# Kernel tuning notes

Measured on AMD Instinct MI355X. Metric: run time of the kernel, lower is better.

## Reference

```python
import jax, jax.numpy as jnp
import numpy as np

B, T, C = 4, 2048, 1024
H, E = 4096, 8


def setup_inputs() -> dict:
    key = jax.random.key(0)
    ks = jax.random.split(key, 6)
    scale = 0.02
    x = jax.random.normal(ks[0], (B, T, C), dtype=jnp.float32)
    w_router = jax.random.normal(ks[1], (C, E), dtype=jnp.float32) * scale
    b_router = jnp.zeros((E,), dtype=jnp.float32)
    w1 = jax.random.normal(ks[2], (E, C, H), dtype=jnp.float32) * scale
    b1 = jnp.zeros((E, H), dtype=jnp.float32)
    w2 = jax.random.normal(ks[3], (E, H, C), dtype=jnp.float32) * scale
    b2 = jnp.zeros((E, C), dtype=jnp.float32)
    return {"x": x, "w_router": w_router, "b_router": b_router,
            "w1": w1, "b1": b1, "w2": w2, "b2": b2}


def reference(x, w_router, b_router, w1, b1, w2, b2):
    # Router: logits -> softmax -> top-1 expert index per token
    logits = jnp.einsum('btc,ce->bte', x, w_router) + b_router  # [B,T,E]
    probs = jax.nn.softmax(logits, axis=-1)
    top1 = jnp.argmax(probs, axis=-1)  # [B,T] int

    # Per-expert dense MLP, combined via top-1 mask (masked scatter in torch).
    out = jnp.zeros_like(x)
    for e in range(E):
        h = jax.nn.gelu(jnp.einsum('btc,ch->bth', x, w1[e]) + b1[e],
                        approximate=False)           # [B,T,H]
        y = jnp.einsum('bth,hc->btc', h, w2[e]) + b2[e]  # [B,T,C]
        out = out + jnp.where((top1 == e)[..., None], y, 0.0)
    return out
```

## Files before the change

### kernel.cpp

```cpp
#include <hip/hip_runtime.h>
#include <cstdint>
#include <cstddef>

#define NTOK 8192
#define C_ 1024
#define H_ 4096
#define E_ 8
#define YMAX2 72

typedef __attribute__((ext_vector_type(8))) short short8;
typedef __attribute__((ext_vector_type(4))) float f32x4;
typedef __attribute__((ext_vector_type(4))) unsigned int u32x4;

__device__ __forceinline__ uint16_t f2b(float f) {
    uint32_t x;
    __builtin_memcpy(&x, &f, 4);
    x = (x + 0x7fffu + ((x >> 16) & 1u)) >> 16;
    return (uint16_t)x;
}

__device__ __forceinline__ float gelu_f(float v) {
    float u = v * (0.7978845608028654f + 0.03567740814183f * v * v);
    float t = __expf(2.f * u);
    float th = 1.f - 2.f / (t + 1.f);
    return 0.5f * v * (1.f + th);
}

__global__ __launch_bounds__(256) void router_kernel(
    const float* __restrict__ x, const float* __restrict__ wr,
    const float* __restrict__ br, int* __restrict__ top1)
{
    int wid = threadIdx.x >> 6, lane = threadIdx.x & 63;
    int tok = blockIdx.x * 4 + wid;
    const float* xrow = x + (size_t)tok * C_;
    float acc[E_];
#pragma unroll
    for (int e = 0; e < E_; e++) acc[e] = 0.f;
#pragma unroll 4
    for (int i = 0; i < C_ / 64; i++) {
        int c = i * 64 + lane;
        float xv = xrow[c];
        const f32x4 w0 = *(const f32x4*)(wr + (size_t)c * E_);
        const f32x4 w1v = *(const f32x4*)(wr + (size_t)c * E_ + 4);
#pragma unroll
        for (int e = 0; e < 4; e++) acc[e] += xv * w0[e];
#pragma unroll
        for (int e = 0; e < 4; e++) acc[4 + e] += xv * w1v[e];
    }
#pragma unroll
    for (int off = 32; off > 0; off >>= 1) {
#pragma unroll
        for (int e = 0; e < E_; e++) acc[e] += __shfl_xor(acc[e], off, 64);
    }
    if (lane == 0) {
        float best = acc[0] + br[0];
        int bi = 0;
#pragma unroll
        for (int e = 1; e < E_; e++) {
            float v = acc[e] + br[e];
            if (v > best) { best = v; bi = e; }
        }
        top1[tok] = bi;
    }
}

__global__ void zero_counts(int* counts) {
    if (threadIdx.x < E_) counts[threadIdx.x] = 0;
}

__global__ __launch_bounds__(1024) void scatter_kernel(
    const int* __restrict__ top1, int* counts, int* __restrict__ idx)
{
    __shared__ int lc[E_], base[E_];
    int tid = threadIdx.x;
    if (tid < E_) lc[tid] = 0;
    __syncthreads();
    int t = blockIdx.x * 1024 + tid;
    int e = top1[t];
    int my = atomicAdd(&lc[e], 1);
    __syncthreads();
    if (tid < E_) base[tid] = atomicAdd(&counts[tid], lc[tid]);
    __syncthreads();
    idx[e * NTOK + base[e] + my] = t;
}

__global__ void plan_kernel(const int* __restrict__ counts,
                            int* __restrict__ tab2, int* __restrict__ ranges2)
{
    if (threadIdx.x == 0) {
        int n = 0, n0 = 0;
        for (int e = 0; e < E_; e++) {
            int nt = (counts[e] + 127) >> 7;
            for (int mb = 0; mb < nt; mb++) tab2[n++] = (e << 16) | mb;
            if (e == 3) n0 = n;
        }
        ranges2[0] = 0;  ranges2[1] = n;
        ranges2[2] = 0;  ranges2[3] = n0;
        ranges2[4] = n0; ranges2[5] = n;
    }
}

__global__ __launch_bounds__(256) void convert_x_kernel(
    const float* __restrict__ x, uint16_t* __restrict__ xb)
{
    size_t i = ((size_t)blockIdx.x * 256 + threadIdx.x) * 8;
    f32x4 a = *(const f32x4*)(x + i);
    f32x4 b = *(const f32x4*)(x + i + 4);
    u32x4 o;
    o.x = (uint32_t)f2b(a.x) | ((uint32_t)f2b(a.y) << 16);
    o.y = (uint32_t)f2b(a.z) | ((uint32_t)f2b(a.w) << 16);
    o.z = (uint32_t)f2b(b.x) | ((uint32_t)f2b(b.y) << 16);
    o.w = (uint32_t)f2b(b.z) | ((uint32_t)f2b(b.w) << 16);
    *(u32x4*)(xb + i) = o;
}

__global__ __launch_bounds__(256) void transpose_cvt_kernel(
    const float* __restrict__ w, uint16_t* __restrict__ wt,
    int K, int N, int ebase)
{
    __shared__ uint16_t tile[64][66];
    int ez = blockIdx.z, e = ebase + ez;
    int n0 = blockIdx.x * 64, k0 = blockIdx.y * 64;
    int t = threadIdx.x;
#pragma unroll
    for (int i = 0; i < 4; i++) {
        int chunk = i * 256 + t;
        int r = chunk >> 4, c4 = chunk & 15;
        f32x4 v = *(const f32x4*)(w + (size_t)(e * K + k0 + r) * N + n0 + c4 * 4);
        uint32_t u0 = (uint32_t)f2b(v.x) | ((uint32_t)f2b(v.y) << 16);
        uint32_t u1 = (uint32_t)f2b(v.z) | ((uint32_t)f2b(v.w) << 16);
        *(uint32_t*)&tile[r][c4 * 4 + 0] = u0;
        *(uint32_t*)&tile[r][c4 * 4 + 2] = u1;
    }
    __syncthreads();
#pragma unroll
    for (int i = 0; i < 2; i++) {
        int chunk = i * 256 + t;
        int rn = chunk >> 3, ck = chunk & 7;
        uint32_t p[4];
#pragma unroll
        for (int j = 0; j < 4; j++) {
            uint32_t lo = tile[ck * 8 + 2 * j][rn];
            uint32_t hi = tile[ck * 8 + 2 * j + 1][rn];
            p[j] = lo | (hi << 16);
        }
        u32x4 v; v.x = p[0]; v.y = p[1]; v.z = p[2]; v.w = p[3];
        *(u32x4*)(wt + ((size_t)ez * N + n0 + rn) * K + k0 + ck * 8) = v;
    }
}

template <int YB, int K, int N, typename OutT, bool GELU>
__global__ __launch_bounds__(256, 3) void gemm_kernel(
    const uint16_t* __restrict__ A, const uint16_t* __restrict__ Bt,
    const float* __restrict__ bias, OutT* __restrict__ Out,
    const int* __restrict__ counts, const int* __restrict__ idx,
    const int* __restrict__ tab, const int* __restrict__ range, int ebase)
{
    constexpr int BM = 128, BN = 128, NW = 256;
    constexpr int MR = 4;
    constexpr int NITER = K / 32;
    constexpr int GX = N / BN;
    constexpr int NWG = GX * YB;
    static_assert(NWG % 8 == 0, "grid must be divisible by 8 XCDs");

    int o = blockIdx.y * GX + blockIdx.x;
    int lid = (o & 7) * (NWG / 8) + (o >> 3);
    int nb = lid % GX;
    int tile = range[0] + lid / GX;
    if (tile >= range[1]) return;
    int ent = tab[tile];
    int e = ent >> 16, mb = ent & 0xffff;
    int ez = e - ebase;
    int cnt = counts[e];

    __shared__ __align__(16) uint16_t As[BM][32];
    __shared__ __align__(16) uint16_t Bs[BN][32];

    int t = threadIdx.x;
    int lane = t & 63, w = t >> 6;
    int wm = w >> 1, wn = w & 1;

    const int* idxe = idx + e * NTOK;

    f32x4 acc[MR][4];
#pragma unroll
    for (int mt = 0; mt < MR; mt++)
#pragma unroll
        for (int nt = 0; nt < 4; nt++) acc[mt][nt] = (f32x4)(0.f);

    const uint16_t* Bte = Bt + ((size_t)ez * N + (size_t)nb * BN) * K;
    uint16_t* As0 = &As[0][0];
    uint16_t* Bs0 = &Bs[0][0];

    const uint16_t* aptr[2];
    const uint16_t* bptr[2];
    uint16_t* adst[2];
    uint16_t* bdst[2];
#pragma unroll
    for (int i = 0; i < 2; i++) {
        int cid = i * NW + t;
        int r = cid >> 2, j = cid & 3;
        int s = mb * BM + r;
        int tk = idxe[(s < cnt) ? s : 0];
        aptr[i] = A + (size_t)tk * K + (j ^ ((r >> 1) & 3)) * 8;
        adst[i] = As0 + (size_t)cid * 8;
    }
#pragma unroll
    for (int i = 0; i < 2; i++) {
        int cid = i * NW + t;
        int r = cid >> 2, j = cid & 3;
        bptr[i] = Bte + (size_t)r * K + (j ^ ((r >> 1) & 3)) * 8;
        bdst[i] = Bs0 + (size_t)cid * 8;
    }

    u32x4 ra[2], rb[2];
    auto loadreg = [&](int kt) {
        int k0 = kt * 32;
#pragma unroll
        for (int i = 0; i < 2; i++) ra[i] = *(const u32x4*)(aptr[i] + k0);
#pragma unroll
        for (int i = 0; i < 2; i++) rb[i] = *(const u32x4*)(bptr[i] + k0);
    };
    auto ldswrite = [&]() {
#pragma unroll
        for (int i = 0; i < 2; i++) *(u32x4*)adst[i] = ra[i];
#pragma unroll
        for (int i = 0; i < 2; i++) *(u32x4*)bdst[i] = rb[i];
    };

    int cs = (((lane >> 4) ^ ((lane & 15) >> 1)) & 3) * 8;

    auto compute = [&]() {
        short8 af[MR], bf[4];
#pragma unroll
        for (int mt = 0; mt < MR; mt++)
            af[mt] = *(const short8*)
                (As0 + (wm * 64 + mt * 16 + (lane & 15)) * 32 + cs);
#pragma unroll
        for (int nt = 0; nt < 4; nt++)
            bf[nt] = *(const short8*)
                (Bs0 + (wn * 64 + nt * 16 + (lane & 15)) * 32 + cs);
#pragma unroll
        for (int mt = 0; mt < MR; mt++)
#pragma unroll
            for (int nt = 0; nt < 4; nt++)
                acc[mt][nt] = __builtin_amdgcn_mfma_f32_16x16x32_bf16(
                    af[mt], bf[nt], acc[mt][nt], 0, 0, 0);
    };

    loadreg(0);
    ldswrite();
    __syncthreads();

    for (int kt = 0; kt < NITER - 1; ++kt) {
        loadreg(kt + 1);
        __builtin_amdgcn_sched_barrier(0);
        compute();
        __syncthreads();
        ldswrite();
        __syncthreads();
    }
    compute();

    const float* be = bias + (size_t)e * N;
#pragma unroll
    for (int mt = 0; mt < MR; mt++) {
        int rbase = wm * 64 + mt * 16 + (lane >> 4) * 4;
#pragma unroll
        for (int r = 0; r < 4; r++) {
            int row = rbase + r;
            int s = mb * BM + row;
            if (s < cnt) {
                int tk = idxe[s];
#pragma unroll
                for (int nt = 0; nt < 4; nt++) {
                    int gcol = nb * BN + wn * 64 + nt * 16 + (lane & 15);
                    float v = acc[mt][nt][r] + be[gcol];
                    if (GELU) v = gelu_f(v);
                    if constexpr (sizeof(OutT) == 2)
                        Out[(size_t)tk * N + gcol] = (OutT)f2b(v);
                    else
                        Out[(size_t)tk * N + gcol] = v;
                }
            }
        }
    }
}

extern "C" void kernel_launch(void* const* d_in, const int* in_sizes, int n_in,
                              void* d_out, int out_size, void* d_ws, size_t ws_size,
                              hipStream_t stream)
{
    const float* x  = (const float*)d_in[0];
    const float* wr = (const float*)d_in[1];
    const float* br = (const float*)d_in[2];
    const float* b1 = (const float*)d_in[4];
    const float* w1 = (const float*)d_in[3];
    const float* w2 = (const float*)d_in[5];
    const float* b2 = (const float*)d_in[6];
    float* out = (float*)d_out;

    char* ws = (char*)d_ws;
    int* counts    = (int*)ws;
    int* top1      = (int*)(ws + 1024);
    int* idx       = (int*)(ws + 64 * 1024);
    int* tab2      = (int*)(ws + 392 * 1024);
    int* ranges2   = (int*)(ws + 396 * 1024);
    uint16_t* xb   = (uint16_t*)(ws + ((size_t)1 << 20));
    uint16_t* hbuf = (uint16_t*)(ws + ((size_t)17 << 20));
    uint16_t* wT   = (uint16_t*)(ws + ((size_t)81 << 20));

    bool big = ws_size >= ((size_t)145 << 20);

    hipLaunchKernelGGL(zero_counts, dim3(1), dim3(64), 0, stream, counts);
    hipLaunchKernelGGL(router_kernel, dim3(NTOK / 4), dim3(256), 0, stream,
                       x, wr, br, top1);
    hipLaunchKernelGGL(scatter_kernel, dim3(NTOK / 1024), dim3(1024), 0, stream,
                       top1, counts, idx);
    hipLaunchKernelGGL(plan_kernel, dim3(1), dim3(64), 0, stream,
                       counts, tab2, ranges2);
    hipLaunchKernelGGL(convert_x_kernel, dim3(NTOK * C_ / (256 * 8)), dim3(256), 0,
                       stream, x, xb);

    if (big) {
        hipLaunchKernelGGL(transpose_cvt_kernel, dim3(H_ / 64, C_ / 64, E_),
                           dim3(256), 0, stream, w1, wT, C_, H_, 0);
        hipLaunchKernelGGL((gemm_kernel<YMAX2, C_, H_, uint16_t, true>),
                           dim3(H_ / 128, YMAX2, 1), dim3(256), 0, stream,
                           xb, wT, b1, hbuf, counts, idx, tab2, ranges2, 0);
        hipLaunchKernelGGL(transpose_cvt_kernel, dim3(C_ / 64, H_ / 64, E_),
                           dim3(256), 0, stream, w2, wT, H_, C_, 0);
        hipLaunchKernelGGL((gemm_kernel<YMAX2, H_, C_, float, false>),
                           dim3(C_ / 128, YMAX2, 1), dim3(256), 0, stream,
                           hbuf, wT, b2, out, counts, idx, tab2, ranges2, 0);
    } else {
        for (int c = 0; c < 2; c++) {
            hipLaunchKernelGGL(transpose_cvt_kernel, dim3(H_ / 64, C_ / 64, 4),
                               dim3(256), 0, stream, w1, wT, C_, H_, c * 4);
            hipLaunchKernelGGL((gemm_kernel<YMAX2, C_, H_, uint16_t, true>),
                               dim3(H_ / 128, YMAX2, 1), dim3(256), 0, stream,
                               xb, wT, b1, hbuf, counts, idx, tab2, ranges2 + 2 + 2 * c, c * 4);
        }
        for (int c = 0; c < 2; c++) {
            hipLaunchKernelGGL(transpose_cvt_kernel, dim3(C_ / 64, H_ / 64, 4),
                               dim3(256), 0, stream, w2, wT, H_, C_, c * 4);
            hipLaunchKernelGGL((gemm_kernel<YMAX2, H_, C_, float, false>),
                               dim3(C_ / 128, YMAX2, 1), dim3(256), 0, stream,
                               hbuf, wT, b2, out, counts, idx, tab2, ranges2 + 2 + 2 * c, c * 4);
        }
    }
}
```

Measured before the change: 570.2 us.

## Template GEMM tile shape and use 256x256x64 tiles for first expert GEMM

```diff
diff --git a/kernel.cpp b/kernel.cpp
--- a/kernel.cpp
+++ b/kernel.cpp
@@ -6,6 +6,7 @@
 #define C_ 1024
 #define H_ 4096
 #define E_ 8
+#define YMAX1 40
 #define YMAX2 72
 
 typedef __attribute__((ext_vector_type(8))) short short8;
@@ -85,10 +86,21 @@
 }
 
 __global__ void plan_kernel(const int* __restrict__ counts,
+                            int* __restrict__ tab1, int* __restrict__ ranges1,
                             int* __restrict__ tab2, int* __restrict__ ranges2)
 {
     if (threadIdx.x == 0) {
         int n = 0, n0 = 0;
+        for (int e = 0; e < E_; e++) {
+            int nt = (counts[e] + 255) >> 8;
+            for (int mb = 0; mb < nt; mb++) tab1[n++] = (e << 16) | mb;
+            if (e == 3) n0 = n;
+        }
+        ranges1[0] = 0;  ranges1[1] = n;
+        ranges1[2] = 0;  ranges1[3] = n0;
+        ranges1[4] = n0; ranges1[5] = n;
+
+        n = 0; n0 = 0;
         for (int e = 0; e < E_; e++) {
             int nt = (counts[e] + 127) >> 7;
             for (int mb = 0; mb < nt; mb++) tab2[n++] = (e << 16) | mb;
@@ -149,19 +161,25 @@
     }
 }
 
-template <int YB, int K, int N, typename OutT, bool GELU>
-__global__ __launch_bounds__(256, 3) void gemm_kernel(
+template <int BM, int BN, int BK, int NW, int WM, int WN, int MINW,
+          int YB, int K, int N, typename OutT, bool GELU>
+__global__ __launch_bounds__(NW, MINW) void gemm_kernel(
     const uint16_t* __restrict__ A, const uint16_t* __restrict__ Bt,
     const float* __restrict__ bias, OutT* __restrict__ Out,
     const int* __restrict__ counts, const int* __restrict__ idx,
     const int* __restrict__ tab, const int* __restrict__ range, int ebase)
 {
-    constexpr int BM = 128, BN = 128, NW = 256;
-    constexpr int MR = 4;
-    constexpr int NITER = K / 32;
+    constexpr int MR = BM / (WM * 16);
+    constexpr int NT = BN / (WN * 16);
+    constexpr int CPR = BK / 8;
+    constexpr int AI = BM * BK / (8 * NW);
+    constexpr int BI = BN * BK / (8 * NW);
+    constexpr int KS = BK / 32;
+    constexpr int NITER = K / BK;
     constexpr int GX = N / BN;
     constexpr int NWG = GX * YB;
     static_assert(NWG % 8 == 0, "grid must be divisible by 8 XCDs");
+    static_assert(CPR == 4 || CPR == 8, "BK must be 32 or 64");
 
     int o = blockIdx.y * GX + blockIdx.x;
     int lid = (o & 7) * (NWG / 8) + (o >> 3);
@@ -173,79 +191,83 @@
     int ez = e - ebase;
     int cnt = counts[e];
 
-    __shared__ __align__(16) uint16_t As[BM][32];
-    __shared__ __align__(16) uint16_t Bs[BN][32];
+    __shared__ __align__(16) uint16_t As[BM][BK];
+    __shared__ __align__(16) uint16_t Bs[BN][BK];
 
     int t = threadIdx.x;
     int lane = t & 63, w = t >> 6;
-    int wm = w >> 1, wn = w & 1;
+    int wm = w / WN, wn = w % WN;
 
     const int* idxe = idx + e * NTOK;
 
-    f32x4 acc[MR][4];
+    f32x4 acc[MR][NT];
 #pragma unroll
     for (int mt = 0; mt < MR; mt++)
 #pragma unroll
-        for (int nt = 0; nt < 4; nt++) acc[mt][nt] = (f32x4)(0.f);
+        for (int nt = 0; nt < NT; nt++) acc[mt][nt] = (f32x4)(0.f);
 
     const uint16_t* Bte = Bt + ((size_t)ez * N + (size_t)nb * BN) * K;
     uint16_t* As0 = &As[0][0];
     uint16_t* Bs0 = &Bs[0][0];
 
-    const uint16_t* aptr[2];
-    const uint16_t* bptr[2];
-    uint16_t* adst[2];
-    uint16_t* bdst[2];
-#pragma unroll
-    for (int i = 0; i < 2; i++) {
+    const uint16_t* aptr[AI];
+    const uint16_t* bptr[BI];
+#pragma unroll
+    for (int i = 0; i < AI; i++) {
         int cid = i * NW + t;
-        int r = cid >> 2, j = cid & 3;
+        int r = cid / CPR, j = cid % CPR;
+        int sw = (CPR == 8) ? (r & 7) : ((r >> 1) & 3);
         int s = mb * BM + r;
         int tk = idxe[(s < cnt) ? s : 0];
-        aptr[i] = A + (size_t)tk * K + (j ^ ((r >> 1) & 3)) * 8;
-        adst[i] = As0 + (size_t)cid * 8;
-    }
-#pragma unroll
-    for (int i = 0; i < 2; i++) {
+        aptr[i] = A + (size_t)tk * K + (j ^ sw) * 8;
+    }
+#pragma unroll
+    for (int i = 0; i < BI; i++) {
         int cid = i * NW + t;
-        int r = cid >> 2, j = cid & 3;
-        bptr[i] = Bte + (size_t)r * K + (j ^ ((r >> 1) & 3)) * 8;
-        bdst[i] = Bs0 + (size_t)cid * 8;
-    }
-
-    u32x4 ra[2], rb[2];
+        int r = cid / CPR, j = cid % CPR;
+        int sw = (CPR == 8) ? (r & 7) : ((r >> 1) & 3);
+        bptr[i] = Bte + (size_t)r * K + (j ^ sw) * 8;
+    }
+
+    u32x4 ra[AI], rb[BI];
     auto loadreg = [&](int kt) {
-        int k0 = kt * 32;
-#pragma unroll
-        for (int i = 0; i < 2; i++) ra[i] = *(const u32x4*)(aptr[i] + k0);
-#pragma unroll
-        for (int i = 0; i < 2; i++) rb[i] = *(const u32x4*)(bptr[i] + k0);
+        int k0 = kt * BK;
+#pragma unroll
+        for (int i = 0; i < AI; i++) ra[i] = *(const u32x4*)(aptr[i] + k0);
+#pragma unroll
+        for (int i = 0; i < BI; i++) rb[i] = *(const u32x4*)(bptr[i] + k0);
     };
     auto ldswrite = [&]() {
 #pragma unroll
-        for (int i = 0; i < 2; i++) *(u32x4*)adst[i] = ra[i];
-#pragma unroll
-        for (int i = 0; i < 2; i++) *(u32x4*)bdst[i] = rb[i];
+        for (int i = 0; i < AI; i++) *(u32x4*)(As0 + (size_t)(i * NW + t) * 8) = ra[i];
+#pragma unroll
+        for (int i = 0; i < BI; i++) *(u32x4*)(Bs0 + (size_t)(i * NW + t) * 8) = rb[i];
     };
 
-    int cs = (((lane >> 4) ^ ((lane & 15) >> 1)) & 3) * 8;
-
     auto compute = [&]() {
-        short8 af[MR], bf[4];
-#pragma unroll
-        for (int mt = 0; mt < MR; mt++)
-            af[mt] = *(const short8*)
-                (As0 + (wm * 64 + mt * 16 + (lane & 15)) * 32 + cs);
-#pragma unroll
-        for (int nt = 0; nt < 4; nt++)
-            bf[nt] = *(const short8*)
-                (Bs0 + (wn * 64 + nt * 16 + (lane & 15)) * 32 + cs);
-#pragma unroll
-        for (int mt = 0; mt < MR; mt++)
-#pragma unroll
-            for (int nt = 0; nt < 4; nt++)
-                acc[mt][nt] = __builtin_amdgcn_mfma_f32_16x16x32_bf16(
-                    af[mt], bf[nt], acc[mt][nt], 0, 0, 0);
+#pragma unroll
+        for (int ks = 0; ks < KS; ks++) {
+            int cs;
+            if constexpr (CPR == 8)
+                cs = (((ks * 4 + (lane >> 4)) ^ (lane & 7)) & 7) * 8;
+            else
+                cs = (((lane >> 4) ^ ((lane & 15) >> 1)) & 3) * 8;
+            short8 af[MR], bf[NT];
+#pragma unroll
+            for (int mt = 0; mt < MR; mt++)
+                af[mt] = *(const short8*)
+                    (As0 + (wm * (BM / WM) + mt * 16 + (lane & 15)) * BK + cs);
+#pragma unroll
+            for (int nt = 0; nt < NT; nt++)
+                bf[nt] = *(const short8*)
+                    (Bs0 + (wn * (BN / WN) + nt * 16 + (lane & 15)) * BK + cs);
+#pragma unroll
+            for (int mt = 0; mt < MR; mt++)
+#pragma unroll
+                for (int nt = 0; nt < NT; nt++)
+                    acc[mt][nt] = __builtin_amdgcn_mfma_f32_16x16x32_bf16(
+                        af[mt], bf[nt], acc[mt][nt], 0, 0, 0);
+        }
     };
 
     loadreg(0);
@@ -265,7 +287,7 @@
     const float* be = bias + (size_t)e * N;
 #pragma unroll
     for (int mt = 0; mt < MR; mt++) {
-        int rbase = wm * 64 + mt * 16 + (lane >> 4) * 4;
+        int rbase = wm * (BM / WM) + mt * 16 + (lane >> 4) * 4;
 #pragma unroll
         for (int r = 0; r < 4; r++) {
             int row = rbase + r;
@@ -273,8 +295,8 @@
             if (s < cnt) {
                 int tk = idxe[s];
 #pragma unroll
-                for (int nt = 0; nt < 4; nt++) {
-                    int gcol = nb * BN + wn * 64 + nt * 16 + (lane & 15);
+                for (int nt = 0; nt < NT; nt++) {
+                    int gcol = nb * BN + wn * (BN / WN) + nt * 16 + (lane & 15);
                     float v = acc[mt][nt][r] + be[gcol];
                     if (GELU) v = gelu_f(v);
                     if constexpr (sizeof(OutT) == 2)
@@ -304,6 +326,8 @@
     int* counts    = (int*)ws;
     int* top1      = (int*)(ws + 1024);
     int* idx       = (int*)(ws + 64 * 1024);
+    int* tab1      = (int*)(ws + 384 * 1024);
+    int* ranges1   = (int*)(ws + 388 * 1024);
     int* tab2      = (int*)(ws + 392 * 1024);
     int* ranges2   = (int*)(ws + 396 * 1024);
     uint16_t* xb   = (uint16_t*)(ws + ((size_t)1 << 20));
@@ -318,33 +342,37 @@
     hipLaunchKernelGGL(scatter_kernel, dim3(NTOK / 1024), dim3(1024), 0, stream,
                        top1, counts, idx);
     hipLaunchKernelGGL(plan_kernel, dim3(1), dim3(64), 0, stream,
-                       counts, tab2, ranges2);
+                       counts, tab1, ranges1, tab2, ranges2);
     hipLaunchKernelGGL(convert_x_kernel, dim3(NTOK * C_ / (256 * 8)), dim3(256), 0,
                        stream, x, xb);
 
     if (big) {
         hipLaunchKernelGGL(transpose_cvt_kernel, dim3(H_ / 64, C_ / 64, E_),
                            dim3(256), 0, stream, w1, wT, C_, H_, 0);
-        hipLaunchKernelGGL((gemm_kernel<YMAX2, C_, H_, uint16_t, true>),
-                           dim3(H_ / 128, YMAX2, 1), dim3(256), 0, stream,
-                           xb, wT, b1, hbuf, counts, idx, tab2, ranges2, 0);
+        hipLaunchKernelGGL((gemm_kernel<256, 256, 64, 512, 2, 4, 2,
+                                        YMAX1, C_, H_, uint16_t, true>),
+                           dim3(H_ / 256, YMAX1, 1), dim3(512), 0, stream,
+                           xb, wT, b1, hbuf, counts, idx, tab1, ranges1, 0);
         hipLaunchKernelGGL(transpose_cvt_kernel, dim3(C_ / 64, H_ / 64, E_),
                            dim3(256), 0, stream, w2, wT, H_, C_, 0);
-        hipLaunchKernelGGL((gemm_kernel<YMAX2, H_, C_, float, false>),
+        hipLaunchKernelGGL((gemm_kernel<128, 128, 32, 256, 2, 2, 6,
+                                        YMAX2, H_, C_, float, false>),
                            dim3(C_ / 128, YMAX2, 1), dim3(256), 0, stream,
                            hbuf, wT, b2, out, counts, idx, tab2, ranges2, 0);
     } else {
         for (int c = 0; c < 2; c++) {
             hipLaunchKernelGGL(transpose_cvt_kernel, dim3(H_ / 64, C_ / 64, 4),
                                dim3(256), 0, stream, w1, wT, C_, H_, c * 4);
-            hipLaunchKernelGGL((gemm_kernel<YMAX2, C_, H_, uint16_t, true>),
-                               dim3(H_ / 128, YMAX2, 1), dim3(256), 0, stream,
-                               xb, wT, b1, hbuf, counts, idx, tab2, ranges2 + 2 + 2 * c, c * 4);
+            hipLaunchKernelGGL((gemm_kernel<256, 256, 64, 512, 2, 4, 2,
+                                            YMAX1, C_, H_, uint16_t, true>),
+                               dim3(H_ / 256, YMAX1, 1), dim3(512), 0, stream,
+                               xb, wT, b1, hbuf, counts, idx, tab1, ranges1 + 2 + 2 * c, c * 4);
         }
         for (int c = 0; c < 2; c++) {
             hipLaunchKernelGGL(transpose_cvt_kernel, dim3(C_ / 64, H_ / 64, 4),
                                dim3(256), 0, stream, w2, wT, H_, C_, c * 4);
-            hipLaunchKernelGGL((gemm_kernel<YMAX2, H_, C_, float, false>),
+            hipLaunchKernelGGL((gemm_kernel<128, 128, 32, 256, 2, 2, 6,
+                                            YMAX2, H_, C_, float, false>),
                                dim3(C_ / 128, YMAX2, 1), dim3(256), 0, stream,
                                hbuf, wT, b2, out, counts, idx, tab2, ranges2 + 2 + 2 * c, c * 4);
         }
```

After: 1.291 ms. 2.26x slower.

## Double-buffer GEMM LDS tiles, fuse x bf16 conversion into router, reorder tile mapping

Applied to the files above, without the earlier changes.

```diff
diff --git a/kernel.cpp b/kernel.cpp
--- a/kernel.cpp
+++ b/kernel.cpp
@@ -6,7 +6,7 @@
 #define C_ 1024
 #define H_ 4096
 #define E_ 8
-#define YMAX2 72
+#define YMAX 72
 
 typedef __attribute__((ext_vector_type(8))) short short8;
 typedef __attribute__((ext_vector_type(4))) float f32x4;
@@ -28,11 +28,13 @@
 
 __global__ __launch_bounds__(256) void router_kernel(
     const float* __restrict__ x, const float* __restrict__ wr,
-    const float* __restrict__ br, int* __restrict__ top1)
+    const float* __restrict__ br, int* __restrict__ top1,
+    uint16_t* __restrict__ xb)
 {
     int wid = threadIdx.x >> 6, lane = threadIdx.x & 63;
     int tok = blockIdx.x * 4 + wid;
     const float* xrow = x + (size_t)tok * C_;
+    uint16_t* xbrow = xb + (size_t)tok * C_;
     float acc[E_];
 #pragma unroll
     for (int e = 0; e < E_; e++) acc[e] = 0.f;
@@ -40,6 +42,7 @@
     for (int i = 0; i < C_ / 64; i++) {
         int c = i * 64 + lane;
         float xv = xrow[c];
+        xbrow[c] = f2b(xv);
         const f32x4 w0 = *(const f32x4*)(wr + (size_t)c * E_);
         const f32x4 w1v = *(const f32x4*)(wr + (size_t)c * E_ + 4);
 #pragma unroll
@@ -85,33 +88,19 @@
 }
 
 __global__ void plan_kernel(const int* __restrict__ counts,
-                            int* __restrict__ tab2, int* __restrict__ ranges2)
+                            int* __restrict__ tab, int* __restrict__ ranges)
 {
     if (threadIdx.x == 0) {
         int n = 0, n0 = 0;
         for (int e = 0; e < E_; e++) {
             int nt = (counts[e] + 127) >> 7;
-            for (int mb = 0; mb < nt; mb++) tab2[n++] = (e << 16) | mb;
+            for (int mb = 0; mb < nt; mb++) tab[n++] = (e << 16) | mb;
             if (e == 3) n0 = n;
         }
-        ranges2[0] = 0;  ranges2[1] = n;
-        ranges2[2] = 0;  ranges2[3] = n0;
-        ranges2[4] = n0; ranges2[5] = n;
-    }
-}
-
-__global__ __launch_bounds__(256) void convert_x_kernel(
-    const float* __restrict__ x, uint16_t* __restrict__ xb)
-{
-    size_t i = ((size_t)blockIdx.x * 256 + threadIdx.x) * 8;
-    f32x4 a = *(const f32x4*)(x + i);
-    f32x4 b = *(const f32x4*)(x + i + 4);
-    u32x4 o;
-    o.x = (uint32_t)f2b(a.x) | ((uint32_t)f2b(a.y) << 16);
-    o.y = (uint32_t)f2b(a.z) | ((uint32_t)f2b(a.w) << 16);
-    o.z = (uint32_t)f2b(b.x) | ((uint32_t)f2b(b.y) << 16);
-    o.w = (uint32_t)f2b(b.z) | ((uint32_t)f2b(b.w) << 16);
-    *(u32x4*)(xb + i) = o;
+        ranges[0] = 0;  ranges[1] = n;
+        ranges[2] = 0;  ranges[3] = n0;
+        ranges[4] = n0; ranges[5] = n;
+    }
 }
 
 __global__ __launch_bounds__(256) void transpose_cvt_kernel(
@@ -162,19 +151,20 @@
     constexpr int GX = N / BN;
     constexpr int NWG = GX * YB;
     static_assert(NWG % 8 == 0, "grid must be divisible by 8 XCDs");
-
-    int o = blockIdx.y * GX + blockIdx.x;
+    static_assert((NITER & 1) == 0, "NITER must be even");
+
+    int o = blockIdx.x * YB + blockIdx.y;
     int lid = (o & 7) * (NWG / 8) + (o >> 3);
-    int nb = lid % GX;
-    int tile = range[0] + lid / GX;
+    int nb = lid / YB;
+    int tile = range[0] + lid % YB;
     if (tile >= range[1]) return;
     int ent = tab[tile];
     int e = ent >> 16, mb = ent & 0xffff;
     int ez = e - ebase;
     int cnt = counts[e];
 
-    __shared__ __align__(16) uint16_t As[BM][32];
-    __shared__ __align__(16) uint16_t Bs[BN][32];
+    __shared__ __align__(16) uint16_t As[2][BM][32];
+    __shared__ __align__(16) uint16_t Bs[2][BN][32];
 
     int t = threadIdx.x;
     int lane = t & 63, w = t >> 6;
@@ -189,13 +179,9 @@
         for (int nt = 0; nt < 4; nt++) acc[mt][nt] = (f32x4)(0.f);
 
     const uint16_t* Bte = Bt + ((size_t)ez * N + (size_t)nb * BN) * K;
-    uint16_t* As0 = &As[0][0];
-    uint16_t* Bs0 = &Bs[0][0];
 
     const uint16_t* aptr[2];
     const uint16_t* bptr[2];
-    uint16_t* adst[2];
-    uint16_t* bdst[2];
 #pragma unroll
     for (int i = 0; i < 2; i++) {
         int cid = i * NW + t;
@@ -203,14 +189,12 @@
         int s = mb * BM + r;
         int tk = idxe[(s < cnt) ? s : 0];
         aptr[i] = A + (size_t)tk * K + (j ^ ((r >> 1) & 3)) * 8;
-        adst[i] = As0 + (size_t)cid * 8;
     }
 #pragma unroll
     for (int i = 0; i < 2; i++) {
         int cid = i * NW + t;
         int r = cid >> 2, j = cid & 3;
         bptr[i] = Bte + (size_t)r * K + (j ^ ((r >> 1) & 3)) * 8;
-        bdst[i] = Bs0 + (size_t)cid * 8;
     }
 
     u32x4 ra[2], rb[2];
@@ -221,25 +205,27 @@
 #pragma unroll
         for (int i = 0; i < 2; i++) rb[i] = *(const u32x4*)(bptr[i] + k0);
     };
-    auto ldswrite = [&]() {
-#pragma unroll
-        for (int i = 0; i < 2; i++) *(u32x4*)adst[i] = ra[i];
-#pragma unroll
-        for (int i = 0; i < 2; i++) *(u32x4*)bdst[i] = rb[i];
+    auto ldswrite = [&](int sel) {
+#pragma unroll
+        for (int i = 0; i < 2; i++)
+            *(u32x4*)(&As[sel][0][0] + (size_t)(i * NW + t) * 8) = ra[i];
+#pragma unroll
+        for (int i = 0; i < 2; i++)
+            *(u32x4*)(&Bs[sel][0][0] + (size_t)(i * NW + t) * 8) = rb[i];
     };
 
     int cs = (((lane >> 4) ^ ((lane & 15) >> 1)) & 3) * 8;
 
-    auto compute = [&]() {
+    auto compute = [&](int sel) {
         short8 af[MR], bf[4];
 #pragma unroll
         for (int mt = 0; mt < MR; mt++)
             af[mt] = *(const short8*)
-                (As0 + (wm * 64 + mt * 16 + (lane & 15)) * 32 + cs);
+                (&As[sel][0][0] + (wm * 64 + mt * 16 + (lane & 15)) * 32 + cs);
 #pragma unroll
         for (int nt = 0; nt < 4; nt++)
             bf[nt] = *(const short8*)
-                (Bs0 + (wn * 64 + nt * 16 + (lane & 15)) * 32 + cs);
+                (&Bs[sel][0][0] + (wn * 64 + nt * 16 + (lane & 15)) * 32 + cs);
 #pragma unroll
         for (int mt = 0; mt < MR; mt++)
 #pragma unroll
@@ -249,18 +235,27 @@
     };
 
     loadreg(0);
-    ldswrite();
-    __syncthreads();
-
-    for (int kt = 0; kt < NITER - 1; ++kt) {
+    ldswrite(0);
+    __syncthreads();
+
+    for (int kt = 0; kt + 2 < NITER; kt += 2) {
         loadreg(kt + 1);
         __builtin_amdgcn_sched_barrier(0);
-        compute();
+        compute(0);
+        ldswrite(1);
         __syncthreads();
-        ldswrite();
+        loadreg(kt + 2);
+        __builtin_amdgcn_sched_barrier(0);
+        compute(1);
+        ldswrite(0);
         __syncthreads();
     }
-    compute();
+    loadreg(NITER - 1);
+    __builtin_amdgcn_sched_barrier(0);
+    compute(0);
+    ldswrite(1);
+    __syncthreads();
+    compute(1);
 
     const float* be = bias + (size_t)e * N;
 #pragma unroll
@@ -304,8 +299,8 @@
     int* counts    = (int*)ws;
     int* top1      = (int*)(ws + 1024);
     int* idx       = (int*)(ws + 64 * 1024);
-    int* tab2      = (int*)(ws + 392 * 1024);
-    int* ranges2   = (int*)(ws + 396 * 1024);
+    int* tab       = (int*)(ws + 392 * 1024);
+    int* ranges    = (int*)(ws + 396 * 1024);
     uint16_t* xb   = (uint16_t*)(ws + ((size_t)1 << 20));
     uint16_t* hbuf = (uint16_t*)(ws + ((size_t)17 << 20));
     uint16_t* wT   = (uint16_t*)(ws + ((size_t)81 << 20));
@@ -314,39 +309,37 @@
 
     hipLaunchKernelGGL(zero_counts, dim3(1), dim3(64), 0, stream, counts);
     hipLaunchKernelGGL(router_kernel, dim3(NTOK / 4), dim3(256), 0, stream,
-                       x, wr, br, top1);
+                       x, wr, br, top1, xb);
     hipLaunchKernelGGL(scatter_kernel, dim3(NTOK / 1024), dim3(1024), 0, stream,
                        top1, counts, idx);
     hipLaunchKernelGGL(plan_kernel, dim3(1), dim3(64), 0, stream,
-                       counts, tab2, ranges2);
-    hipLaunchKernelGGL(convert_x_kernel, dim3(NTOK * C_ / (256 * 8)), dim3(256), 0,
-                       stream, x, xb);
+                       counts, tab, ranges);
 
     if (big) {
         hipLaunchKernelGGL(transpose_cvt_kernel, dim3(H_ / 64, C_ / 64, E_),
                            dim3(256), 0, stream, w1, wT, C_, H_, 0);
-        hipLaunchKernelGGL((gemm_kernel<YMAX2, C_, H_, uint16_t, true>),
-                           dim3(H_ / 128, YMAX2, 1), dim3(256), 0, stream,
-                           xb, wT, b1, hbuf, counts, idx, tab2, ranges2, 0);
+        hipLaunchKernelGGL((gemm_kernel<YMAX, C_, H_, uint16_t, true>),
+                           dim3(H_ / 128, YMAX, 1), dim3(256), 0, stream,
+                           xb, wT, b1, hbuf, counts, idx, tab, ranges, 0);
         hipLaunchKernelGGL(transpose_cvt_kernel, dim3(C_ / 64, H_ / 64, E_),
                            dim3(256), 0, stream, w2, wT, H_, C_, 0);
-        hipLaunchKernelGGL((gemm_kernel<YMAX2, H_, C_, float, false>),
-                           dim3(C_ / 128, YMAX2, 1), dim3(256), 0, stream,
-                           hbuf, wT, b2, out, counts, idx, tab2, ranges2, 0);
+        hipLaunchKernelGGL((gemm_kernel<YMAX, H_, C_, float, false>),
+                           dim3(C_ / 128, YMAX, 1), dim3(256), 0, stream,
+                           hbuf, wT, b2, out, counts, idx, tab, ranges, 0);
     } else {
         for (int c = 0; c < 2; c++) {
             hipLaunchKernelGGL(transpose_cvt_kernel, dim3(H_ / 64, C_ / 64, 4),
                                dim3(256), 0, stream, w1, wT, C_, H_, c * 4);
-            hipLaunchKernelGGL((gemm_kernel<YMAX2, C_, H_, uint16_t, true>),
-                               dim3(H_ / 128, YMAX2, 1), dim3(256), 0, stream,
-                               xb, wT, b1, hbuf, counts, idx, tab2, ranges2 + 2 + 2 * c, c * 4);
+            hipLaunchKernelGGL((gemm_kernel<YMAX, C_, H_, uint16_t, true>),
+                               dim3(H_ / 128, YMAX, 1), dim3(256), 0, stream,
+                               xb, wT, b1, hbuf, counts, idx, tab, ranges + 2 + 2 * c, c * 4);
         }
         for (int c = 0; c < 2; c++) {
             hipLaunchKernelGGL(transpose_cvt_kernel, dim3(C_ / 64, H_ / 64, 4),
                                dim3(256), 0, stream, w2, wT, H_, C_, c * 4);
-            hipLaunchKernelGGL((gemm_kernel<YMAX2, H_, C_, float, false>),
-                               dim3(C_ / 128, YMAX2, 1), dim3(256), 0, stream,
-                               hbuf, wT, b2, out, counts, idx, tab2, ranges2 + 2 + 2 * c, c * 4);
-        }
-    }
-}
+            hipLaunchKernelGGL((gemm_kernel<YMAX, H_, C_, float, false>),
+                               dim3(C_ / 128, YMAX, 1), dim3(256), 0, stream,
+                               hbuf, wT, b2, out, counts, idx, tab, ranges + 2 + 2 * c, c * 4);
+        }
+    }
+}
```

New measurement: 568.2 us. Within noise of the previous version (-0.3%).
